# Kernel tuning notes

Measured on AMD Instinct MI355X. Metric: run time of the kernel, lower is better.

Reference implementation:

```python
import jax, jax.numpy as jnp
import numpy as np

B, C, H, W = 2, 3, 96, 96
OC = 2  # conv output channels
EPS = 1e-5

def setup_inputs() -> dict:
    key = jax.random.key(0)
    k1, k2, k3, k4 = jax.random.split(key, 4)
    return {
        "X_tnext": jax.random.normal(k1, (B, C, H, W), dtype=jnp.float32),
        "X_hat_tnext": jax.random.normal(k2, (B, C, H, W), dtype=jnp.float32),
        "conv_w": jax.random.normal(k3, (OC, C, 3, 3), dtype=jnp.float32) * 0.1,
        "conv_b": jax.random.normal(k4, (OC,), dtype=jnp.float32) * 0.1,
        "gamma": jnp.ones((OC,), dtype=jnp.float32),
        "beta": jnp.zeros((OC,), dtype=jnp.float32),
    }

def reference(X_tnext, X_hat_tnext, conv_w, conv_b, gamma, beta):
    b, c, h, w = X_tnext.shape
    n = h * w
    q = X_tnext.reshape(b, c, n)
    k = X_hat_tnext.reshape(b, c, n)
    # corr4D: [b, n, n] = q^T k / sqrt(c)  (materialized O(N^2) volume, as in source)
    corr = jnp.einsum('bcn,bcm->bnm', q, k) / jnp.sqrt(jnp.asarray(c, jnp.float32))
    # weighted aggregation: corr @ X_tnext (broadcast over channels)
    agg = jnp.einsum('bnm,bcm->bcn', corr, q).reshape(b, c, h, w)
    # Conv2d(3->2, k=3, s=1, p=1)
    y = jax.lax.conv_general_dilated(
        agg, conv_w, window_strides=(1, 1), padding='SAME',
        dimension_numbers=('NCHW', 'OIHW', 'NCHW'))
    y = y + conv_b[None, :, None, None]
    # BatchNorm2d (training-mode batch statistics, biased var, eps=1e-5)
    mean = jnp.mean(y, axis=(0, 2, 3), keepdims=True)
    var = jnp.var(y, axis=(0, 2, 3), keepdims=True)
    y = (y - mean) * jax.lax.rsqrt(var + EPS)
    y = y * gamma[None, :, None, None] + beta[None, :, None, None]
    # LeakyReLU(0.1)
    return jnp.where(y >= 0, y, 0.1 * y)
```

## Files before the change

kernel.cpp:

```cpp
#include <hip/hip_runtime.h>
#include <math.h>

namespace {
constexpr int kB = 2, kC = 3, kOC = 2, kH = 96, kW = 96;
constexpr int kN      = kH * kW;
constexpr int kChunks = kN / 256;
constexpr int kBlocks = kB * kChunks;
constexpr float kEps   = 1e-5f;
constexpr float kScale = 0.57735026918962576f;
constexpr int WS_P     = 0;
constexpr int WS_CTR_B = 1280;
}

__global__ __launch_bounds__(256) void k_fused(const float* __restrict__ X,
                                               const float* __restrict__ Xh,
                                               const float* __restrict__ cw,
                                               const float* __restrict__ cb,
                                               const float* __restrict__ gamma,
                                               const float* __restrict__ beta,
                                               float* __restrict__ ws,
                                               float* __restrict__ out) {
    const int tid = threadIdx.x;
    const int blk = blockIdx.x;
    const int b   = blk / kChunks;
    const int pix = (blk % kChunks) * 256 + tid;
    const int h = pix / kW, w = pix % kW;

    const float*  qb  = X  + (size_t)b * kC * kN;
    const float4* qb4 = (const float4*)qb;
    const float4* kb4 = (const float4*)(Xh + (size_t)b * kC * kN);

    float m[9] = {0,0,0,0,0,0,0,0,0};
    #pragma unroll
    for (int it = 0; it < 9; ++it) {
        const int n = it * 256 + tid;
        const float4 q0 = qb4[n], q1 = qb4[kN/4 + n], q2 = qb4[2*kN/4 + n];
        const float4 k0 = kb4[n], k1 = kb4[kN/4 + n], k2 = kb4[2*kN/4 + n];
        m[0] += k0.x*q0.x + k0.y*q0.y + k0.z*q0.z + k0.w*q0.w;
        m[1] += k0.x*q1.x + k0.y*q1.y + k0.z*q1.z + k0.w*q1.w;
        m[2] += k0.x*q2.x + k0.y*q2.y + k0.z*q2.z + k0.w*q2.w;
        m[3] += k1.x*q0.x + k1.y*q0.y + k1.z*q0.z + k1.w*q0.w;
        m[4] += k1.x*q1.x + k1.y*q1.y + k1.z*q1.z + k1.w*q1.w;
        m[5] += k1.x*q2.x + k1.y*q2.y + k1.z*q2.z + k1.w*q2.w;
        m[6] += k2.x*q0.x + k2.y*q0.y + k2.z*q0.z + k2.w*q0.w;
        m[7] += k2.x*q1.x + k2.y*q1.y + k2.z*q1.z + k2.w*q1.w;
        m[8] += k2.x*q2.x + k2.y*q2.y + k2.z*q2.z + k2.w*q2.w;
    }

    float qt0[9], qt1[9], qt2[9];
    #pragma unroll
    for (int dh = 0; dh < 3; ++dh) {
        #pragma unroll
        for (int dw = 0; dw < 3; ++dw) {
            const int hh = h + dh - 1, ww = w + dw - 1;
            const bool ok = (hh >= 0) && (hh < kH) && (ww >= 0) && (ww < kW);
            const int p = ok ? hh * kW + ww : pix;
            const int t = dh * 3 + dw;
            const float f0 = qb[p], f1 = qb[kN + p], f2 = qb[2 * kN + p];
            qt0[t] = ok ? f0 : 0.f;
            qt1[t] = ok ? f1 : 0.f;
            qt2[t] = ok ? f2 : 0.f;
        }
    }

    #pragma unroll
    for (int off = 32; off > 0; off >>= 1) {
        #pragma unroll
        for (int j = 0; j < 9; ++j) m[j] += __shfl_down(m[j], off);
    }
    __shared__ float sMw[4][9];
    __shared__ float sM[9];
    __shared__ float sE[2][3][9];
    if ((tid & 63) == 0) {
        #pragma unroll
        for (int j = 0; j < 9; ++j) sMw[tid >> 6][j] = m[j];
    }
    __syncthreads();
    if (tid < 9) sM[tid] = sMw[0][tid] + sMw[1][tid] + sMw[2][tid] + sMw[3][tid];
    __syncthreads();
    if (tid < 54) {
        const int oc = tid / 27, r = tid % 27, cp = r / 9, nb = r % 9;
        sE[oc][cp][nb] = kScale * (cw[oc * 27 +      nb] * sM[cp * 3 + 0] +
                                   cw[oc * 27 +  9 + nb] * sM[cp * 3 + 1] +
                                   cw[oc * 27 + 18 + nb] * sM[cp * 3 + 2]);
    }
    __syncthreads();

    float acc0 = cb[0], acc1 = cb[1];
    #pragma unroll
    for (int t = 0; t < 9; ++t) {
        acc0 += qt0[t] * sE[0][0][t] + qt1[t] * sE[0][1][t] + qt2[t] * sE[0][2][t];
        acc1 += qt0[t] * sE[1][0][t] + qt1[t] * sE[1][1][t] + qt2[t] * sE[1][2][t];
    }

    float v0 = acc0, v1 = acc0 * acc0, v2 = acc1, v3 = acc1 * acc1;
    #pragma unroll
    for (int off = 32; off > 0; off >>= 1) {
        v0 += __shfl_down(v0, off); v1 += __shfl_down(v1, off);
        v2 += __shfl_down(v2, off); v3 += __shfl_down(v3, off);
    }
    __shared__ float sP[4][4];
    if ((tid & 63) == 0) {
        const int wv = tid >> 6;
        sP[wv][0] = v0; sP[wv][1] = v1; sP[wv][2] = v2; sP[wv][3] = v3;
    }
    __syncthreads();
    if (tid < 4)
        ws[WS_P + blk * 4 + tid] = sP[0][tid] + sP[1][tid] + sP[2][tid] + sP[3][tid];

    __syncthreads();
    unsigned int* ctr = (unsigned int*)((char*)ws + WS_CTR_B);
    if (tid == 0) {
        __threadfence();
        __hip_atomic_fetch_add(ctr, 1u, __ATOMIC_ACQ_REL, __HIP_MEMORY_SCOPE_AGENT);
        while (__hip_atomic_load(ctr, __ATOMIC_ACQUIRE, __HIP_MEMORY_SCOPE_AGENT) < (unsigned)kBlocks)
            __builtin_amdgcn_s_sleep(1);
    }
    __syncthreads();
    __threadfence();

    const int lane = tid & 63;
    const float4* P4 = (const float4*)(ws + WS_P);
    float4 s = P4[lane];
    if (lane < kBlocks - 64) {
        const float4 e = P4[64 + lane];
        s.x += e.x; s.y += e.y; s.z += e.z; s.w += e.w;
    }
    #pragma unroll
    for (int off = 32; off > 0; off >>= 1) {
        s.x += __shfl_xor(s.x, off);
        s.y += __shfl_xor(s.y, off);
        s.z += __shfl_xor(s.z, off);
        s.w += __shfl_xor(s.w, off);
    }
    const float inv   = 1.f / (float)(kB * kN);
    const float mean0 = s.x * inv, mean1 = s.z * inv;
    const float g0 = gamma[0] * rsqrtf(s.y * inv - mean0 * mean0 + kEps);
    const float g1 = gamma[1] * rsqrtf(s.w * inv - mean1 * mean1 + kEps);
    const float y0 = (acc0 - mean0) * g0 + beta[0];
    const float y1 = (acc1 - mean1) * g1 + beta[1];
    out[(size_t)(b * kOC + 0) * kN + pix] = (y0 >= 0.f) ? y0 : 0.1f * y0;
    out[(size_t)(b * kOC + 1) * kN + pix] = (y1 >= 0.f) ? y1 : 0.1f * y1;
}

extern "C" void kernel_launch(void* const* d_in, const int* in_sizes, int n_in,
                              void* d_out, int out_size, void* d_ws, size_t ws_size,
                              hipStream_t stream) {
    const float* X      = (const float*)d_in[0];
    const float* Xhat   = (const float*)d_in[1];
    const float* conv_w = (const float*)d_in[2];
    const float* conv_b = (const float*)d_in[3];
    const float* gamma  = (const float*)d_in[4];
    const float* beta   = (const float*)d_in[5];
    float* ws = (float*)d_ws;

    hipMemsetAsync((char*)d_ws + WS_CTR_B, 0, 4, stream);
    k_fused<<<kBlocks, 256, 0, stream>>>(X, Xhat, conv_w, conv_b, gamma, beta,
                                         ws, (float*)d_out);
}
```

Before: 78.20 us.

## Split fused kernel into conv and BN kernels, replacing the atomic grid barrier

The single fused kernel used a memset plus an atomic spin-wait grid barrier before applying batch-norm statistics. It is now two kernels. The first computes the conv output, stores it to workspace, and writes per-block partial sums. The second reads those values, reduces the statistics and applies BN plus LeakyReLU. The conv-weight folding also moves from a shared-memory precompute with extra syncs to per-thread register arithmetic. This removes the memset launch and the spin barrier, at the cost of an extra kernel launch, a workspace round trip for the conv output, and more per-thread FLOPs.

Result: faster. 71.35 us (-8.8%).

```diff
diff --git a/kernel.cpp b/kernel.cpp
--- a/kernel.cpp
+++ b/kernel.cpp
@@ -1,5 +1,6 @@
 #include <hip/hip_runtime.h>
 #include <math.h>
+
 
 namespace {
 constexpr int kB = 2, kC = 3, kOC = 2, kH = 96, kW = 96;
@@ -8,18 +9,15 @@
 constexpr int kBlocks = kB * kChunks;
 constexpr float kEps   = 1e-5f;
 constexpr float kScale = 0.57735026918962576f;
-constexpr int WS_P     = 0;
-constexpr int WS_CTR_B = 1280;
+constexpr int WS_P = 0;
+constexpr int WS_Y = 512;
 }
 
-__global__ __launch_bounds__(256) void k_fused(const float* __restrict__ X,
+__global__ __launch_bounds__(256) void kA_conv(const float* __restrict__ X,
                                                const float* __restrict__ Xh,
                                                const float* __restrict__ cw,
                                                const float* __restrict__ cb,
-                                               const float* __restrict__ gamma,
-                                               const float* __restrict__ beta,
-                                               float* __restrict__ ws,
-                                               float* __restrict__ out) {
+                                               float* __restrict__ ws) {
     const int tid = threadIdx.x;
     const int blk = blockIdx.x;
     const int b   = blk / kChunks;
@@ -69,29 +67,35 @@
         for (int j = 0; j < 9; ++j) m[j] += __shfl_down(m[j], off);
     }
     __shared__ float sMw[4][9];
-    __shared__ float sM[9];
-    __shared__ float sE[2][3][9];
     if ((tid & 63) == 0) {
         #pragma unroll
         for (int j = 0; j < 9; ++j) sMw[tid >> 6][j] = m[j];
     }
     __syncthreads();
-    if (tid < 9) sM[tid] = sMw[0][tid] + sMw[1][tid] + sMw[2][tid] + sMw[3][tid];
-    __syncthreads();
-    if (tid < 54) {
-        const int oc = tid / 27, r = tid % 27, cp = r / 9, nb = r % 9;
-        sE[oc][cp][nb] = kScale * (cw[oc * 27 +      nb] * sM[cp * 3 + 0] +
-                                   cw[oc * 27 +  9 + nb] * sM[cp * 3 + 1] +
-                                   cw[oc * 27 + 18 + nb] * sM[cp * 3 + 2]);
-    }
-    __syncthreads();
+    float M[9];
+    #pragma unroll
+    for (int j = 0; j < 9; ++j)
+        M[j] = sMw[0][j] + sMw[1][j] + sMw[2][j] + sMw[3][j];
 
-    float acc0 = cb[0], acc1 = cb[1];
+    float S[3][9];
     #pragma unroll
     for (int t = 0; t < 9; ++t) {
-        acc0 += qt0[t] * sE[0][0][t] + qt1[t] * sE[0][1][t] + qt2[t] * sE[0][2][t];
-        acc1 += qt0[t] * sE[1][0][t] + qt1[t] * sE[1][1][t] + qt2[t] * sE[1][2][t];
+        #pragma unroll
+        for (int ic = 0; ic < 3; ++ic)
+            S[ic][t] = qt0[t] * M[ic] + qt1[t] * M[3 + ic] + qt2[t] * M[6 + ic];
     }
+    float t0 = 0.f, t1 = 0.f;
+    #pragma unroll
+    for (int ic = 0; ic < 3; ++ic) {
+        #pragma unroll
+        for (int t = 0; t < 9; ++t) {
+            t0 += cw[     ic * 9 + t] * S[ic][t];
+            t1 += cw[27 + ic * 9 + t] * S[ic][t];
+        }
+    }
+    const float acc0 = cb[0] + kScale * t0;
+    const float acc1 = cb[1] + kScale * t1;
+    ((float2*)(ws + WS_Y))[(size_t)b * kN + pix] = make_float2(acc0, acc1);
 
     float v0 = acc0, v1 = acc0 * acc0, v2 = acc1, v3 = acc1 * acc1;
     #pragma unroll
@@ -107,19 +111,20 @@
     __syncthreads();
     if (tid < 4)
         ws[WS_P + blk * 4 + tid] = sP[0][tid] + sP[1][tid] + sP[2][tid] + sP[3][tid];
+}
 
-    __syncthreads();
-    unsigned int* ctr = (unsigned int*)((char*)ws + WS_CTR_B);
-    if (tid == 0) {
-        __threadfence();
-        __hip_atomic_fetch_add(ctr, 1u, __ATOMIC_ACQ_REL, __HIP_MEMORY_SCOPE_AGENT);
-        while (__hip_atomic_load(ctr, __ATOMIC_ACQUIRE, __HIP_MEMORY_SCOPE_AGENT) < (unsigned)kBlocks)
-            __builtin_amdgcn_s_sleep(1);
-    }
-    __syncthreads();
-    __threadfence();
+__global__ __launch_bounds__(256) void kB_bn(const float* __restrict__ ws,
+                                             const float* __restrict__ gamma,
+                                             const float* __restrict__ beta,
+                                             float* __restrict__ out) {
+    const int tid = threadIdx.x;
+    const int blk = blockIdx.x;
+    const int b   = blk / kChunks;
+    const int pix = (blk % kChunks) * 256 + tid;
+    const int lane = tid & 63;
 
-    const int lane = tid & 63;
+    const float2 y2 = ((const float2*)(ws + WS_Y))[(size_t)b * kN + pix];
+
     const float4* P4 = (const float4*)(ws + WS_P);
     float4 s = P4[lane];
     if (lane < kBlocks - 64) {
@@ -137,8 +142,8 @@
     const float mean0 = s.x * inv, mean1 = s.z * inv;
     const float g0 = gamma[0] * rsqrtf(s.y * inv - mean0 * mean0 + kEps);
     const float g1 = gamma[1] * rsqrtf(s.w * inv - mean1 * mean1 + kEps);
-    const float y0 = (acc0 - mean0) * g0 + beta[0];
-    const float y1 = (acc1 - mean1) * g1 + beta[1];
+    const float y0 = (y2.x - mean0) * g0 + beta[0];
+    const float y1 = (y2.y - mean1) * g1 + beta[1];
     out[(size_t)(b * kOC + 0) * kN + pix] = (y0 >= 0.f) ? y0 : 0.1f * y0;
     out[(size_t)(b * kOC + 1) * kN + pix] = (y1 >= 0.f) ? y1 : 0.1f * y1;
 }
@@ -154,7 +159,6 @@
     const float* beta   = (const float*)d_in[5];
     float* ws = (float*)d_ws;
 
-    hipMemsetAsync((char*)d_ws + WS_CTR_B, 0, 4, stream);
-    k_fused<<<kBlocks, 256, 0, stream>>>(X, Xhat, conv_w, conv_b, gamma, beta,
-                                         ws, (float*)d_out);
+    kA_conv<<<kBlocks, 256, 0, stream>>>(X, Xhat, conv_w, conv_b, ws);
+    kB_bn  <<<kBlocks, 256, 0, stream>>>(ws, gamma, beta, (float*)d_out);
 }
```
